# Optimization experiments

Hardware: AMD Instinct MI355X
Metric: run time of the kernel (lower is better)

## Reference

```python
import jax, jax.numpy as jnp
import numpy as np

ALPHA = 2.0
EPS = 1e-12  # F.normalize default eps


def setup_inputs() -> dict:
    key = jax.random.key(0)
    k1, k2 = jax.random.split(key)
    x = jax.random.normal(k1, (16, 512, 48, 48), dtype=jnp.float32)
    # 1x1 conv weight [out=1, in=C, 1, 1] flattened to [C], xavier-like scale
    w_query = jax.random.normal(k2, (512,), dtype=jnp.float32) * (2.0 / (512 + 1)) ** 0.5
    return {"x": x, "w_query": w_query}


def reference(x, w_query):
    b, c, h, w = x.shape
    n = h * w
    # attention map from detached x: 1x1 conv (dot over channels) + softplus -> [b, n]
    xd = jax.lax.stop_gradient(x)
    att = jax.nn.softplus(jnp.einsum('bchw,c->bhw', xd, w_query)).reshape(b, n)
    # L2-normalize over channel dim, flatten spatial -> [b, c, n]
    norm = jnp.sqrt(jnp.sum(x * x, axis=1, keepdims=True))
    flat = (x / jnp.maximum(norm, EPS)).reshape(b, c, n)
    # full NxN similarity, relu^alpha
    sim = jnp.einsum('bcn,bcm->bnm', flat, flat)  # [b, n, n]
    score = jnp.maximum(sim, 0.0) ** ALPHA
    # combine with attention map -> refine score per spatial location
    refine = jnp.einsum('bnm,bm->bn', score, att).reshape(b, 1, h, w)
    # weighted global average pool -> [b, c, 1, 1]
    return jnp.mean(x * refine, axis=(2, 3), keepdims=True)
```

## Files before the change

### kernel.cpp

```cpp
#include <hip/hip_runtime.h>

#define C_DIM 512
#define N_PIX 2304
#define B_DIM 16
#define K8    (C_DIM / 8)
#define K8_STRIDE (N_PIX * 8)
#define FB_STRIDE ((size_t)K8 * K8_STRIDE)
#define NB (B_DIM * N_PIX)

typedef float floatx4 __attribute__((ext_vector_type(4)));
typedef __bf16 bf16x8 __attribute__((ext_vector_type(8)));

static __device__ __forceinline__ unsigned short f2bf(float f) {
    unsigned u = __float_as_uint(f);
    return (unsigned short)((u + 0x7fffu + ((u >> 16) & 1u)) >> 16);
}

static __device__ __forceinline__ float softplus_stable(float z) {
    return (z > 0.f) ? (z + log1pf(expf(-z))) : log1pf(expf(z));
}

static __device__ __forceinline__ void load_lds16(const void* gp, void* l) {
    __builtin_amdgcn_global_load_lds(
        (const __attribute__((address_space(1))) unsigned int*)gp,
        (__attribute__((address_space(3))) unsigned int*)l, 16, 0, 0);
}

__global__ __launch_bounds__(256) void xcvt_kernel(const float* __restrict__ x,
                                                   const float* __restrict__ w,
                                                   unsigned short* __restrict__ F,
                                                   float* __restrict__ accd,
                                                   float* __restrict__ accs) {
    const int pg = blockIdx.x;
    const int cg = blockIdx.y;
    const int b  = pg / 9;
    const int p  = (pg - b * 9) * 256 + threadIdx.x;
    const float* xb = x + (size_t)b * C_DIM * N_PIX + p;

    float dot = 0.f, sq = 0.f;
    #pragma unroll
    for (int k8l = 0; k8l < 4; ++k8l) {
        const int k8 = cg * 4 + k8l;
        float v[8];
        #pragma unroll
        for (int kk = 0; kk < 8; ++kk)
            v[kk] = xb[(size_t)(k8 * 8 + kk) * N_PIX];
        union { unsigned short u[8]; int4 q; } cell;
        #pragma unroll
        for (int kk = 0; kk < 8; ++kk) {
            dot = fmaf(v[kk], w[k8 * 8 + kk], dot);
            sq  = fmaf(v[kk], v[kk], sq);
            cell.u[kk] = f2bf(v[kk]);
        }
        *(int4*)(F + (size_t)b * FB_STRIDE + (size_t)k8 * K8_STRIDE + (size_t)p * 8) = cell.q;
    }
    atomicAdd(&accd[b * N_PIX + p], dot);
    atomicAdd(&accs[b * N_PIX + p], sq);
}

__global__ __launch_bounds__(256) void finalize_kernel(const float* __restrict__ accd,
                                                       const float* __restrict__ accs,
                                                       float* __restrict__ g,
                                                       float* __restrict__ rn2,
                                                       float* __restrict__ refine) {
    const int bp = blockIdx.x * 256 + threadIdx.x;
    const float d = accd[bp];
    const float s = accs[bp];
    const float r2 = 1.0f / fmaxf(s, 1e-24f);
    g[bp]      = softplus_stable(d) * r2;
    rn2[bp]    = r2;
    refine[bp] = 0.f;
}

__global__ __launch_bounds__(256) void refine_kernel(const unsigned short* __restrict__ F,
                                                     const float* __restrict__ g,
                                                     float* __restrict__ refine) {
    const int id   = blockIdx.x;
    const int xcd  = id & 7;
    const int slot = id >> 3;
    const int hi   = (slot >= 171) ? 1 : 0;
    const int b    = xcd + 8 * hi;
    int t = slot - 171 * hi, bi = 0;
    while (t >= 18 - bi) { t -= 18 - bi; ++bi; }
    const int bj = bi + t;
    const int n0 = bi * 128;
    const int m0 = bj * 128;
    const bool mirror = (bi != bj);

    const unsigned short* Fb = F + (size_t)b * FB_STRIDE;
    const float* gb = g + b * N_PIX;

    __shared__ __align__(16) unsigned short As[4 * 128 * 8];
    __shared__ __align__(16) unsigned short Bs[4 * 128 * 8];

    const int tid  = threadIdx.x;
    const int lane = tid & 63;
    const int wave = tid >> 6;
    const int wr = wave >> 1, wc = wave & 1;
    const int quad = lane >> 4, lcol = lane & 15;

    floatx4 acc[4][4];
    #pragma unroll
    for (int i = 0; i < 4; ++i)
        #pragma unroll
        for (int j = 0; j < 4; ++j)
            acc[i][j] = (floatx4)0.f;

    const unsigned short* gA = Fb + (size_t)wave * K8_STRIDE + (size_t)n0 * 8 + lane * 8;
    const unsigned short* gB = Fb + (size_t)wave * K8_STRIDE + (size_t)m0 * 8 + lane * 8;

    for (int ck = 0; ck < 16; ++ck) {
        const unsigned short* sA = gA + (size_t)ck * (4 * K8_STRIDE);
        const unsigned short* sB = gB + (size_t)ck * (4 * K8_STRIDE);
        __syncthreads();
        load_lds16(sA,       &As[wave * 1024]);
        load_lds16(sA + 512, &As[wave * 1024 + 512]);
        load_lds16(sB,       &Bs[wave * 1024]);
        load_lds16(sB + 512, &Bs[wave * 1024 + 512]);
        __syncthreads();

        bf16x8 af[4], bfr[4];
        #pragma unroll
        for (int mi = 0; mi < 4; ++mi)
            af[mi] = *(const bf16x8*)&As[(quad * 128 + wr * 64 + mi * 16 + lcol) * 8];
        #pragma unroll
        for (int ni = 0; ni < 4; ++ni)
            bfr[ni] = *(const bf16x8*)&Bs[(quad * 128 + wc * 64 + ni * 16 + lcol) * 8];
        #pragma unroll
        for (int mi = 0; mi < 4; ++mi)
            #pragma unroll
            for (int ni = 0; ni < 4; ++ni)
                acc[mi][ni] = __builtin_amdgcn_mfma_f32_16x16x32_bf16(af[mi], bfr[ni], acc[mi][ni], 0, 0, 0);
    }

    float gC[4];
    #pragma unroll
    for (int ni = 0; ni < 4; ++ni)
        gC[ni] = gb[m0 + wc * 64 + ni * 16 + lcol];

    #pragma unroll
    for (int mi = 0; mi < 4; ++mi) {
        float part[4] = {0.f, 0.f, 0.f, 0.f};
        #pragma unroll
        for (int ni = 0; ni < 4; ++ni) {
            #pragma unroll
            for (int r = 0; r < 4; ++r) {
                float s = fmaxf(acc[mi][ni][r], 0.f);
                part[r] = fmaf(s * s, gC[ni], part[r]);
            }
        }
        #pragma unroll
        for (int r = 0; r < 4; ++r) {
            float v = part[r];
            v += __shfl_xor(v, 1);
            v += __shfl_xor(v, 2);
            v += __shfl_xor(v, 4);
            v += __shfl_xor(v, 8);
            if (lcol == 0)
                atomicAdd(&refine[b * N_PIX + n0 + wr * 64 + mi * 16 + quad * 4 + r], v);
        }
    }

    if (mirror) {
        float gR[4][4];
        #pragma unroll
        for (int mi = 0; mi < 4; ++mi)
            #pragma unroll
            for (int r = 0; r < 4; ++r)
                gR[mi][r] = gb[n0 + wr * 64 + mi * 16 + quad * 4 + r];

        #pragma unroll
        for (int ni = 0; ni < 4; ++ni) {
            float msum = 0.f;
            #pragma unroll
            for (int mi = 0; mi < 4; ++mi) {
                #pragma unroll
                for (int r = 0; r < 4; ++r) {
                    float s = fmaxf(acc[mi][ni][r], 0.f);
                    msum = fmaf(s * s, gR[mi][r], msum);
                }
            }
            msum += __shfl_xor(msum, 16);
            msum += __shfl_xor(msum, 32);
            if (quad == 0)
                atomicAdd(&refine[b * N_PIX + m0 + wc * 64 + ni * 16 + lcol], msum);
        }
    }
}

__global__ __launch_bounds__(256) void pool_kernel(const unsigned short* __restrict__ F,
                                                   const float* __restrict__ refine,
                                                   const float* __restrict__ rn2,
                                                   float* __restrict__ out) {
    const int lane = threadIdx.x & 63;
    const int wave = threadIdx.x >> 6;
    const int b  = blockIdx.x >> 6;
    const int k8 = blockIdx.x & 63;
    const unsigned short* Fr = F + (size_t)b * FB_STRIDE + (size_t)k8 * K8_STRIDE;
    const float* rf = refine + b * N_PIX;
    const float* r2 = rn2 + b * N_PIX;
    float s[8] = {0.f, 0.f, 0.f, 0.f, 0.f, 0.f, 0.f, 0.f};
    #pragma unroll
    for (int j = 0; j < 9; ++j) {
        const int n = (j * 4 + wave) * 64 + lane;
        bf16x8 fv = *(const bf16x8*)(Fr + (size_t)n * 8);
        float rr = rf[n] * r2[n];
        #pragma unroll
        for (int kk = 0; kk < 8; ++kk)
            s[kk] = fmaf((float)fv[kk], rr, s[kk]);
    }
    __shared__ float sred[4][8];
    #pragma unroll
    for (int kk = 0; kk < 8; ++kk) {
        float v = s[kk];
        #pragma unroll
        for (int off = 32; off > 0; off >>= 1) v += __shfl_down(v, off);
        if (lane == 0) sred[wave][kk] = v;
    }
    __syncthreads();
    if (threadIdx.x < 8) {
        const int kk = threadIdx.x;
        out[b * C_DIM + k8 * 8 + kk] =
            (sred[0][kk] + sred[1][kk] + sred[2][kk] + sred[3][kk]) * (1.0f / N_PIX);
    }
}

__global__ __launch_bounds__(256) void prep_kernel(const float* __restrict__ x,
                                                   const float* __restrict__ w,
                                                   float* __restrict__ rnorm,
                                                   float* __restrict__ att) {
    const int tid = threadIdx.x;
    const int px = tid & 63;
    const int cc = tid >> 6;
    const int pglob = blockIdx.x * 64 + px;
    const int b = pglob / N_PIX;
    const int p = pglob - b * N_PIX;

    const float* xb = x + (size_t)b * C_DIM * N_PIX + p;
    float dot = 0.f, sq = 0.f;
    #pragma unroll 4
    for (int c = cc * 128; c < cc * 128 + 128; ++c) {
        float v = xb[(size_t)c * N_PIX];
        dot = fmaf(v, w[c], dot);
        sq  = fmaf(v, v, sq);
    }
    __shared__ float sdot[4][64];
    __shared__ float ssq[4][64];
    sdot[cc][px] = dot;
    ssq[cc][px]  = sq;
    __syncthreads();
    if (cc == 0) {
        dot = sdot[0][px] + sdot[1][px] + sdot[2][px] + sdot[3][px];
        sq  = ssq[0][px]  + ssq[1][px]  + ssq[2][px]  + ssq[3][px];
        att[pglob] = softplus_stable(dot);
        rnorm[pglob] = 1.0f / fmaxf(sqrtf(sq), 1e-12f);
    }
}

__global__ __launch_bounds__(256) void refine_fallback(const float* __restrict__ x,
                                                       const float* __restrict__ rnorm,
                                                       const float* __restrict__ att,
                                                       float* __restrict__ refine) {
    const int b  = blockIdx.z;
    const int n0 = blockIdx.x * 128;
    const int m0 = blockIdx.y * 128;
    const float* xb = x + (size_t)b * C_DIM * N_PIX;
    const float* rn = rnorm + b * N_PIX;
    const float* ab = att + b * N_PIX;

    __shared__ __align__(16) unsigned short As[4 * 128 * 8];
    __shared__ __align__(16) unsigned short Bs[4 * 128 * 8];

    const int tid  = threadIdx.x;
    const int nl   = tid & 127;
    const int half = tid >> 7;
    const int lane = tid & 63;
    const int wave = tid >> 6;
    const int wr = wave >> 1, wc = wave & 1;
    const int quad = lane >> 4, lcol = lane & 15;

    const float rA = rn[n0 + nl];
    const float rB = rn[m0 + nl];

    floatx4 acc[4][4];
    #pragma unroll
    for (int i = 0; i < 4; ++i)
        #pragma unroll
        for (int j = 0; j < 4; ++j)
            acc[i][j] = (floatx4)0.f;

    for (int k0 = 0; k0 < C_DIM; k0 += 32) {
        const float* xa = xb + (size_t)(k0 + half * 16) * N_PIX;
        union { unsigned short u[16]; int4 v[2]; } ta, tb;
        #pragma unroll
        for (int j = 0; j < 16; ++j) {
            float va = xa[(size_t)j * N_PIX + n0 + nl];
            float vb = xa[(size_t)j * N_PIX + m0 + nl];
            ta.u[j] = f2bf(va * rA);
            tb.u[j] = f2bf(vb * rB);
        }
        __syncthreads();
        *(int4*)&As[((half * 2 + 0) * 128 + nl) * 8] = ta.v[0];
        *(int4*)&As[((half * 2 + 1) * 128 + nl) * 8] = ta.v[1];
        *(int4*)&Bs[((half * 2 + 0) * 128 + nl) * 8] = tb.v[0];
        *(int4*)&Bs[((half * 2 + 1) * 128 + nl) * 8] = tb.v[1];
        __syncthreads();

        bf16x8 af[4], bfr[4];
        #pragma unroll
        for (int mi = 0; mi < 4; ++mi)
            af[mi] = *(const bf16x8*)&As[(quad * 128 + wr * 64 + mi * 16 + lcol) * 8];
        #pragma unroll
        for (int ni = 0; ni < 4; ++ni)
            bfr[ni] = *(const bf16x8*)&Bs[(quad * 128 + wc * 64 + ni * 16 + lcol) * 8];
        #pragma unroll
        for (int mi = 0; mi < 4; ++mi)
            #pragma unroll
            for (int ni = 0; ni < 4; ++ni)
                acc[mi][ni] = __builtin_amdgcn_mfma_f32_16x16x32_bf16(af[mi], bfr[ni], acc[mi][ni], 0, 0, 0);
    }

    float attv[4];
    #pragma unroll
    for (int ni = 0; ni < 4; ++ni)
        attv[ni] = ab[m0 + wc * 64 + ni * 16 + lcol];

    #pragma unroll
    for (int mi = 0; mi < 4; ++mi) {
        float part[4] = {0.f, 0.f, 0.f, 0.f};
        #pragma unroll
        for (int ni = 0; ni < 4; ++ni) {
            #pragma unroll
            for (int r = 0; r < 4; ++r) {
                float s = fmaxf(acc[mi][ni][r], 0.f);
                part[r] = fmaf(s * s, attv[ni], part[r]);
            }
        }
        #pragma unroll
        for (int r = 0; r < 4; ++r) {
            float v = part[r];
            v += __shfl_xor(v, 1);
            v += __shfl_xor(v, 2);
            v += __shfl_xor(v, 4);
            v += __shfl_xor(v, 8);
            if (lcol == 0)
                atomicAdd(&refine[b * N_PIX + n0 + wr * 64 + mi * 16 + quad * 4 + r], v);
        }
    }
}

__global__ __launch_bounds__(256) void pool_fallback(const float* __restrict__ x,
                                                     const float* __restrict__ refine,
                                                     float* __restrict__ out) {
    const int lane = threadIdx.x & 63;
    const int wave = threadIdx.x >> 6;
    const int gidx = blockIdx.x * 4 + wave;
    const int b = gidx >> 9;
    const float4* xr = (const float4*)(x + (size_t)gidx * N_PIX);
    const float4* rr = (const float4*)(refine + (size_t)b * N_PIX);
    float s = 0.f;
    #pragma unroll
    for (int j = 0; j < 9; ++j) {
        float4 xv = xr[j * 64 + lane];
        float4 rv = rr[j * 64 + lane];
        s += xv.x * rv.x + xv.y * rv.y + xv.z * rv.z + xv.w * rv.w;
    }
    #pragma unroll
    for (int off = 32; off > 0; off >>= 1) s += __shfl_down(s, off);
    if (lane == 0) out[gidx] = s * (1.0f / N_PIX);
}

extern "C" void kernel_launch(void* const* d_in, const int* in_sizes, int n_in,
                              void* d_out, int out_size, void* d_ws, size_t ws_size,
                              hipStream_t stream) {
    const float* x = (const float*)d_in[0];
    const float* w = (const float*)d_in[1];
    float* rn2    = (float*)d_ws;
    float* g      = rn2 + NB;
    float* refine = g + NB;
    float* accd   = refine + NB;
    float* accs   = accd + NB;
    unsigned short* F = (unsigned short*)(accs + NB);
    float* out    = (float*)d_out;

    const size_t need = (size_t)5 * NB * 4 + (size_t)B_DIM * FB_STRIDE * 2;

    if (ws_size >= need) {
        hipMemsetAsync(accd, 0, (size_t)2 * NB * 4, stream);
        xcvt_kernel<<<dim3(144, 16), 256, 0, stream>>>(x, w, F, accd, accs);
        finalize_kernel<<<dim3(144), 256, 0, stream>>>(accd, accs, g, rn2, refine);
        refine_kernel<<<dim3(171 * 16), 256, 0, stream>>>(F, g, refine);
        pool_kernel<<<dim3(B_DIM * K8), 256, 0, stream>>>(F, refine, rn2, out);
    } else {
        hipMemsetAsync(refine, 0, (size_t)NB * 4, stream);
        prep_kernel<<<dim3(NB / 64), 256, 0, stream>>>(x, w, rn2, g);
        refine_fallback<<<dim3(18, 18, B_DIM), 256, 0, stream>>>(x, rn2, g, refine);
        pool_fallback<<<dim3(B_DIM * C_DIM / 4), 256, 0, stream>>>(x, refine, out);
    }
}
```

Measured before the change: 183.5 us.

## Vectorize conversion kernel and replace atomics with per-slice partial sums

The x-to-bf16 conversion kernel now has each thread load float4 spans of four pixels and write four packed bf16 cells. Per-block channel partial dot and sum-of-squares are reduced in shared memory and written to eight slice buffers, which the finalize kernel then sums. This removes the global atomics and the memset launch. In exchange it uses more workspace and adds extra reads in finalize.

```diff
diff --git a/kernel.cpp b/kernel.cpp
--- a/kernel.cpp
+++ b/kernel.cpp
@@ -7,6 +7,7 @@
 #define K8_STRIDE (N_PIX * 8)
 #define FB_STRIDE ((size_t)K8 * K8_STRIDE)
 #define NB (B_DIM * N_PIX)
+#define NSLICE 8
 
 typedef float floatx4 __attribute__((ext_vector_type(4)));
 typedef __bf16 bf16x8 __attribute__((ext_vector_type(8)));
@@ -33,29 +34,55 @@
                                                    float* __restrict__ accs) {
     const int pg = blockIdx.x;
     const int cg = blockIdx.y;
-    const int b  = pg / 9;
-    const int p  = (pg - b * 9) * 256 + threadIdx.x;
-    const float* xb = x + (size_t)b * C_DIM * N_PIX + p;
-
-    float dot = 0.f, sq = 0.f;
-    #pragma unroll
-    for (int k8l = 0; k8l < 4; ++k8l) {
-        const int k8 = cg * 4 + k8l;
-        float v[8];
-        #pragma unroll
-        for (int kk = 0; kk < 8; ++kk)
-            v[kk] = xb[(size_t)(k8 * 8 + kk) * N_PIX];
-        union { unsigned short u[8]; int4 q; } cell;
-        #pragma unroll
-        for (int kk = 0; kk < 8; ++kk) {
-            dot = fmaf(v[kk], w[k8 * 8 + kk], dot);
-            sq  = fmaf(v[kk], v[kk], sq);
-            cell.u[kk] = f2bf(v[kk]);
-        }
-        *(int4*)(F + (size_t)b * FB_STRIDE + (size_t)k8 * K8_STRIDE + (size_t)p * 8) = cell.q;
-    }
-    atomicAdd(&accd[b * N_PIX + p], dot);
-    atomicAdd(&accs[b * N_PIX + p], sq);
+    const int b  = pg / 18;
+    const int p0 = (pg - b * 18) * 128;
+    const int tid = threadIdx.x;
+    const int p4  = tid & 31;
+    const int k8g = tid >> 5;
+    const int k8  = cg * 8 + k8g;
+    const int p   = p0 + p4 * 4;
+
+    const float* xb = x + (size_t)b * C_DIM * N_PIX;
+    float4 d4 = {0.f, 0.f, 0.f, 0.f};
+    float4 s4 = {0.f, 0.f, 0.f, 0.f};
+    union { unsigned short u[4][8]; int4 v[4]; } cell;
+
+    #pragma unroll
+    for (int kk = 0; kk < 8; ++kk) {
+        float4 xv = *(const float4*)(xb + (size_t)(k8 * 8 + kk) * N_PIX + p);
+        const float wc = w[k8 * 8 + kk];
+        d4.x = fmaf(xv.x, wc, d4.x);  s4.x = fmaf(xv.x, xv.x, s4.x);
+        d4.y = fmaf(xv.y, wc, d4.y);  s4.y = fmaf(xv.y, xv.y, s4.y);
+        d4.z = fmaf(xv.z, wc, d4.z);  s4.z = fmaf(xv.z, xv.z, s4.z);
+        d4.w = fmaf(xv.w, wc, d4.w);  s4.w = fmaf(xv.w, xv.w, s4.w);
+        cell.u[0][kk] = f2bf(xv.x);
+        cell.u[1][kk] = f2bf(xv.y);
+        cell.u[2][kk] = f2bf(xv.z);
+        cell.u[3][kk] = f2bf(xv.w);
+    }
+    unsigned short* dst = F + (size_t)b * FB_STRIDE + (size_t)k8 * K8_STRIDE + (size_t)p * 8;
+    #pragma unroll
+    for (int i = 0; i < 4; ++i)
+        *(int4*)(dst + i * 8) = cell.v[i];
+
+    __shared__ float4 sd[NSLICE][32];
+    __shared__ float4 ss[NSLICE][32];
+    sd[k8g][p4] = d4;
+    ss[k8g][p4] = s4;
+    __syncthreads();
+
+    if (tid < 32) {
+        float4 d = sd[0][tid], s = ss[0][tid];
+        #pragma unroll
+        for (int j = 1; j < NSLICE; ++j) {
+            float4 dj = sd[j][tid], sj = ss[j][tid];
+            d.x += dj.x; d.y += dj.y; d.z += dj.z; d.w += dj.w;
+            s.x += sj.x; s.y += sj.y; s.z += sj.z; s.w += sj.w;
+        }
+        const int o = b * N_PIX + p0 + tid * 4;
+        *(float4*)(accd + (size_t)cg * NB + o) = d;
+        *(float4*)(accs + (size_t)cg * NB + o) = s;
+    }
 }
 
 __global__ __launch_bounds__(256) void finalize_kernel(const float* __restrict__ accd,
@@ -64,8 +91,12 @@
                                                        float* __restrict__ rn2,
                                                        float* __restrict__ refine) {
     const int bp = blockIdx.x * 256 + threadIdx.x;
-    const float d = accd[bp];
-    const float s = accs[bp];
+    float d = 0.f, s = 0.f;
+    #pragma unroll
+    for (int i = 0; i < NSLICE; ++i) {
+        d += accd[(size_t)i * NB + bp];
+        s += accs[(size_t)i * NB + bp];
+    }
     const float r2 = 1.0f / fmaxf(s, 1e-24f);
     g[bp]      = softplus_stable(d) * r2;
     rn2[bp]    = r2;
@@ -379,16 +410,15 @@
     float* g      = rn2 + NB;
     float* refine = g + NB;
     float* accd   = refine + NB;
-    float* accs   = accd + NB;
-    unsigned short* F = (unsigned short*)(accs + NB);
+    float* accs   = accd + (size_t)NSLICE * NB;
+    unsigned short* F = (unsigned short*)(accs + (size_t)NSLICE * NB);
     float* out    = (float*)d_out;
 
-    const size_t need = (size_t)5 * NB * 4 + (size_t)B_DIM * FB_STRIDE * 2;
+    const size_t need = (size_t)(3 + 2 * NSLICE) * NB * 4 + (size_t)B_DIM * FB_STRIDE * 2;
 
     if (ws_size >= need) {
-        hipMemsetAsync(accd, 0, (size_t)2 * NB * 4, stream);
-        xcvt_kernel<<<dim3(144, 16), 256, 0, stream>>>(x, w, F, accd, accs);
-        finalize_kernel<<<dim3(144), 256, 0, stream>>>(accd, accs, g, rn2, refine);
+        xcvt_kernel<<<dim3(288, NSLICE), 256, 0, stream>>>(x, w, F, accd, accs);
+        finalize_kernel<<<dim3(NB / 256), 256, 0, stream>>>(accd, accs, g, rn2, refine);
         refine_kernel<<<dim3(171 * 16), 256, 0, stream>>>(F, g, refine);
         pool_kernel<<<dim3(B_DIM * K8), 256, 0, stream>>>(F, refine, rn2, out);
     } else {
```

Result: slower. 188.8 us (+2.8%).
